# Optimization experiments

Measured on AMD Instinct MI355X. Metric: run time of the kernel, lower is better.

The kernel has to match this reference:

```python
import jax, jax.numpy as jnp
import numpy as np

EPS = 1e-12  # F.normalize default eps


def _sage_conv(x, src, dst, num_nodes, W_l, W_r, b):
    # mean-aggregate neighbor features: for each dst node, mean over x[src]
    agg = jax.ops.segment_sum(x[src], dst, num_segments=num_nodes)  # [N, d_in]
    cnt = jax.ops.segment_sum(jnp.ones((src.shape[0],), x.dtype), dst,
                              num_segments=num_nodes)
    mean = agg / jnp.maximum(cnt, 1.0)[:, None]
    # PyG SAGEConv: lin_l(aggregated) + bias + lin_r(root)
    return mean @ W_l + b + x @ W_r


def setup_inputs() -> dict:
    key = jax.random.key(0)
    ks = jax.random.split(key, 10)
    N, E, F_in = 50000, 400000, 128
    x = jax.random.normal(ks[0], (N, F_in), dtype=jnp.float32)
    edge_index = jax.random.randint(ks[1], (2, E), 0, N, dtype=jnp.int64)

    def lin(k, din, dout):
        s = 1.0 / np.sqrt(din)
        return jax.random.uniform(k, (din, dout), jnp.float32, -s, s)

    params = {
        "W1_l": lin(ks[2], F_in, 2048), "W1_r": lin(ks[3], F_in, 2048),
        "b1": jnp.zeros((2048,), jnp.float32),
        "W2_l": lin(ks[4], 2048, 2048), "W2_r": lin(ks[5], 2048, 2048),
        "b2": jnp.zeros((2048,), jnp.float32),
        "W3_l": lin(ks[6], 2048, 1024), "W3_r": lin(ks[7], 2048, 1024),
        "b3": jnp.zeros((1024,), jnp.float32),
    }
    return {"x": x, "unused": 0, "edge_index": edge_index, **params}


def reference(x, unused, edge_index,
              W1_l, W1_r, b1, W2_l, W2_r, b2, W3_l, W3_r, b3):
    del unused
    N = x.shape[0]
    src, dst = edge_index[0], edge_index[1]
    h = jax.nn.relu(_sage_conv(x, src, dst, N, W1_l, W1_r, b1))
    h = jax.nn.relu(_sage_conv(h, src, dst, N, W2_l, W2_r, b2))
    h = jax.nn.relu(_sage_conv(h, src, dst, N, W3_l, W3_r, b3))
    # F.normalize(dim=1): x / max(||x||_2, eps)
    norm = jnp.linalg.norm(h, axis=1, keepdims=True)
    return h / jnp.maximum(norm, EPS)
```

## Files before the change

### kernel.cpp

```cpp
#include <hip/hip_runtime.h>
#include <stdint.h>

#define NN 50000
#define EE 400000

typedef unsigned short u16;
typedef __attribute__((ext_vector_type(8))) short bf16x8;
typedef __attribute__((ext_vector_type(4))) float f32x4;
typedef __attribute__((address_space(3))) uint32_t lds_u32_t;
typedef __attribute__((address_space(1))) uint32_t glob_u32_t;

__device__ inline float bf2f(u16 u) {
  union { uint32_t i; float f; } x; x.i = ((uint32_t)u) << 16; return x.f;
}
__device__ inline u16 f2bf(float f) {
  union { float f; uint32_t i; } x; x.f = f;
  x.i += 0x7fffu + ((x.i >> 16) & 1u);
  return (u16)(x.i >> 16);
}
__device__ inline void gload_lds16(const void* g, void* l) {
  __builtin_amdgcn_global_load_lds((const glob_u32_t*)g, (lds_u32_t*)l, 16, 0, 0);
}

__global__ void detect_i64(const int* __restrict__ e, int* __restrict__ flag) {
  __shared__ int sh[256];
  int t = threadIdx.x;
  int v = 0;
  for (int i = t; i < 4096; i += 256) v |= e[2 * i + 1];
  sh[t] = v; __syncthreads();
  for (int s = 128; s > 0; s >>= 1) { if (t < s) sh[t] |= sh[t + s]; __syncthreads(); }
  if (t == 0) flag[0] = (sh[0] == 0) ? 1 : 0;
}

__global__ void conv_edges(const int* __restrict__ e, const int* __restrict__ flag,
                           int* __restrict__ src, int* __restrict__ dst) {
  int i = blockIdx.x * 256 + threadIdx.x;
  if (i >= EE) return;
  if (flag[0]) { src[i] = e[2 * i]; dst[i] = e[2 * (EE + i)]; }
  else         { src[i] = e[i];     dst[i] = e[EE + i]; }
}

__global__ void count_edges(const int* __restrict__ dst, int* __restrict__ cnt) {
  int i = blockIdx.x * 256 + threadIdx.x;
  if (i < EE) atomicAdd(&cnt[dst[i]], 1);
}

__global__ void scan_counts(const int* __restrict__ cnt, int* __restrict__ offs,
                            int* __restrict__ cursor) {
  __shared__ int sh[1024];
  __shared__ int carry_sh;
  int tid = threadIdx.x;
  if (tid == 0) carry_sh = 0;
  __syncthreads();
  int nChunks = (NN + 1023) / 1024;
  for (int c = 0; c < nChunks; ++c) {
    int idx = c * 1024 + tid;
    int v = (idx < NN) ? cnt[idx] : 0;
    sh[tid] = v; __syncthreads();
    for (int off = 1; off < 1024; off <<= 1) {
      int t = (tid >= off) ? sh[tid - off] : 0;
      __syncthreads();
      sh[tid] += t;
      __syncthreads();
    }
    int incl = sh[tid];
    int excl = incl - v + carry_sh;
    if (idx < NN) { offs[idx] = excl; cursor[idx] = excl; }
    __syncthreads();
    if (tid == 0) carry_sh += sh[1023];
    __syncthreads();
  }
}

__global__ void fill_buckets(const int* __restrict__ src, const int* __restrict__ dst,
                             int* __restrict__ cursor, int* __restrict__ bucket) {
  int i = blockIdx.x * 256 + threadIdx.x;
  if (i >= EE) return;
  int p = atomicAdd(&cursor[dst[i]], 1);
  bucket[p] = src[i];
}

__global__ void cvt_bf16(const float* __restrict__ in, u16* __restrict__ out, int n4) {
  int i = blockIdx.x * 256 + threadIdx.x;
  if (i >= n4) return;
  float4 v = ((const float4*)in)[i];
  u16 o[4] = { f2bf(v.x), f2bf(v.y), f2bf(v.z), f2bf(v.w) };
  uint2 pack;
  pack.x = (uint32_t)o[0] | ((uint32_t)o[1] << 16);
  pack.y = (uint32_t)o[2] | ((uint32_t)o[3] << 16);
  ((uint2*)out)[i] = pack;
}

__global__ void transposeW(const float* __restrict__ W, u16* __restrict__ Wt,
                           int K, int Nc) {
  __shared__ float tile[32][33];
  int n0 = blockIdx.x * 32, k0 = blockIdx.y * 32;
  int tx = threadIdx.x, ty = threadIdx.y;
  #pragma unroll
  for (int i = 0; i < 4; ++i)
    tile[ty + i * 8][tx] = W[(size_t)(k0 + ty + i * 8) * Nc + n0 + tx];
  __syncthreads();
  #pragma unroll
  for (int i = 0; i < 4; ++i)
    Wt[(size_t)(n0 + ty + i * 8) * K + k0 + tx] = f2bf(tile[tx][ty + i * 8]);
}

template<int D>
__global__ void agg_mean(const u16* __restrict__ h, const int* __restrict__ offs,
                         const int* __restrict__ cnt, const int* __restrict__ bucket,
                         u16* __restrict__ outp) {
  int node = blockIdx.x;
  int t = threadIdx.x;
  int base = t * 8;
  if (base >= D) return;
  int start = offs[node];
  int c = cnt[node];
  float acc[8];
  #pragma unroll
  for (int i = 0; i < 8; ++i) acc[i] = 0.f;
  for (int j = 0; j < c; ++j) {
    int s = bucket[start + j];
    uint4 q = *(const uint4*)(h + (size_t)s * D + base);
    acc[0] += bf2f((u16)(q.x & 0xffff)); acc[1] += bf2f((u16)(q.x >> 16));
    acc[2] += bf2f((u16)(q.y & 0xffff)); acc[3] += bf2f((u16)(q.y >> 16));
    acc[4] += bf2f((u16)(q.z & 0xffff)); acc[5] += bf2f((u16)(q.z >> 16));
    acc[6] += bf2f((u16)(q.w & 0xffff)); acc[7] += bf2f((u16)(q.w >> 16));
  }
  float inv = 1.0f / fmaxf((float)c, 1.0f);
  uint4 o;
  o.x = (uint32_t)f2bf(acc[0] * inv) | ((uint32_t)f2bf(acc[1] * inv) << 16);
  o.y = (uint32_t)f2bf(acc[2] * inv) | ((uint32_t)f2bf(acc[3] * inv) << 16);
  o.z = (uint32_t)f2bf(acc[4] * inv) | ((uint32_t)f2bf(acc[5] * inv) << 16);
  o.w = (uint32_t)f2bf(acc[6] * inv) | ((uint32_t)f2bf(acc[7] * inv) << 16);
  *(uint4*)(outp + (size_t)node * D + base) = o;
}


template<int K>
__device__ inline void stage_half(char* ldsX, const u16* __restrict__ G, int grow0,
                                  int k0, int h, int wave, int lrow8, int slot8,
                                  int clampR) {
  #pragma unroll
  for (int j = 0; j < 2; ++j) {
    const int lrow = h * 128 + j * 64 + wave * 8;
    int gr = grow0 + lrow + lrow8;
    gr = gr < clampR ? gr : clampR - 1;
    gload_lds16(G + (size_t)gr * K + k0 + slot8, ldsX + lrow * 128);
  }
}

#define LOAD_A(MH)                                                              \
  _Pragma("unroll") for (int mf = 0; mf < 4; ++mf) {                            \
    af[mf][0] = *(const bf16x8*)(cA + ((MH) * 128 + mf * 16) * 128 + kc0);      \
    af[mf][1] = *(const bf16x8*)(cA + ((MH) * 128 + mf * 16) * 128 + kc1);      \
  }
#define LOAD_B(DST, NH)                                                         \
  _Pragma("unroll") for (int nf = 0; nf < 2; ++nf) {                            \
    DST[nf][0] = *(const bf16x8*)(cB + ((NH) * 128 + nf * 16) * 128 + kc0);     \
    DST[nf][1] = *(const bf16x8*)(cB + ((NH) * 128 + nf * 16) * 128 + kc1);     \
  }
#define QUAD(MH, BREG, NH)                                                      \
  _Pragma("unroll") for (int mf = 0; mf < 4; ++mf)                              \
  _Pragma("unroll") for (int nf = 0; nf < 2; ++nf) {                            \
    acc[(MH)*4+mf][(NH)*2+nf] = __builtin_amdgcn_mfma_f32_16x16x32_bf16(        \
        af[mf][0], BREG[nf][0], acc[(MH)*4+mf][(NH)*2+nf], 0, 0, 0);            \
    acc[(MH)*4+mf][(NH)*2+nf] = __builtin_amdgcn_mfma_f32_16x16x32_bf16(        \
        af[mf][1], BREG[nf][1], acc[(MH)*4+mf][(NH)*2+nf], 0, 0, 0);            \
  }

template<int K, bool OUT_F32>
__global__ __launch_bounds__(512, 2)
void gemm8ph(const u16* __restrict__ A1, const u16* __restrict__ A2,
             const u16* __restrict__ B1t, const u16* __restrict__ B2t,
             const float* __restrict__ bias, void* __restrict__ Cout,
             int M, int Nc, int tilesN) {
  __shared__ __align__(16) char lds[131072];
  constexpr int NTp = K / 64;
  constexpr int NT = 2 * NTp;

  const int nwg = gridDim.x;
  const int bid = blockIdx.x;
  const int wg = (bid & 7) * (nwg >> 3) + (bid >> 3);
  const int bx = wg % tilesN, by = wg / tilesN;
  const int rowBase = by * 256, colBase = bx * 256;

  const int tid = threadIdx.x;
  const int lane = tid & 63;
  const int wave = tid >> 6;
  const int wm = wave >> 2, wn = wave & 3;
  const int r = lane & 15, kg = lane >> 4;
  const int sw = (r & 7) << 4;
  const int kc0 = (kg * 16) ^ sw;
  const int kc1 = (64 + kg * 16) ^ sw;
  const int slot8 = ((lane & 7) ^ ((lane >> 3) & 7)) * 8;
  const int lrow8 = lane >> 3;

  char* const pA0 = lds + (wm * 64 + r) * 128;
  char* const pB0 = lds + 32768 + (wn * 32 + r) * 128;

  f32x4 acc[8][4];
  #pragma unroll
  for (int m = 0; m < 8; ++m)
    #pragma unroll
    for (int n = 0; n < 4; ++n) acc[m][n] = (f32x4){0.f, 0.f, 0.f, 0.f};

  bf16x8 af[4][2], b0[2][2], b1[2][2];

  stage_half<K>(lds,         A1,  rowBase, 0, 0, wave, lrow8, slot8, M);
  stage_half<K>(lds + 32768, B1t, colBase, 0, 0, wave, lrow8, slot8, Nc);
  stage_half<K>(lds + 32768, B1t, colBase, 0, 1, wave, lrow8, slot8, Nc);
  stage_half<K>(lds,         A1,  rowBase, 0, 1, wave, lrow8, slot8, M);
  asm volatile("s_waitcnt vmcnt(4)" ::: "memory");
  __builtin_amdgcn_s_barrier();

  for (int t = 0; t < NT; ++t) {
    const int cur = t & 1;
    const char* cA = pA0 + cur * 65536;
    const char* cB = pB0 + cur * 65536;
    char* nA = lds + (cur ^ 1) * 65536;
    char* nB = nA + 32768;
    const int vt = (t + 1 < NT) ? t + 1 : NT - 1;
    const u16* sA; const u16* sB; int sk0;
    if (vt >= NTp) { sA = A2; sB = B2t; sk0 = (vt - NTp) * 64; }
    else           { sA = A1; sB = B1t; sk0 = vt * 64; }

    LOAD_A(0); LOAD_B(b0, 0);
    stage_half<K>(nA, sA, rowBase, sk0, 0, wave, lrow8, slot8, M);
    __builtin_amdgcn_s_barrier();
    asm volatile("s_waitcnt lgkmcnt(0)" ::: "memory");
    __builtin_amdgcn_s_setprio(1);
    QUAD(0, b0, 0);
    __builtin_amdgcn_s_setprio(0);
    asm volatile("s_waitcnt vmcnt(4)" ::: "memory");
    __builtin_amdgcn_s_barrier();

    LOAD_B(b1, 1);
    stage_half<K>(nB, sB, colBase, sk0, 0, wave, lrow8, slot8, Nc);
    __builtin_amdgcn_s_barrier();
    asm volatile("s_waitcnt lgkmcnt(0)" ::: "memory");
    __builtin_amdgcn_s_setprio(1);
    QUAD(0, b1, 1);
    __builtin_amdgcn_s_setprio(0);
    asm volatile("s_waitcnt vmcnt(4)" ::: "memory");
    __builtin_amdgcn_s_barrier();

    LOAD_A(1);
    stage_half<K>(nB, sB, colBase, sk0, 1, wave, lrow8, slot8, Nc);
    __builtin_amdgcn_s_barrier();
    asm volatile("s_waitcnt lgkmcnt(0)" ::: "memory");
    __builtin_amdgcn_s_setprio(1);
    QUAD(1, b1, 1);
    __builtin_amdgcn_s_setprio(0);
    __builtin_amdgcn_s_barrier();

    stage_half<K>(nA, sA, rowBase, sk0, 1, wave, lrow8, slot8, M);
    __builtin_amdgcn_s_barrier();
    __builtin_amdgcn_s_setprio(1);
    QUAD(1, b0, 0);
    __builtin_amdgcn_s_setprio(0);
    asm volatile("s_waitcnt vmcnt(4)" ::: "memory");
    __builtin_amdgcn_s_barrier();
  }

  asm volatile("s_waitcnt vmcnt(0)" ::: "memory");

  const int q = lane >> 4;
  #pragma unroll
  for (int m = 0; m < 8; ++m) {
    int row = rowBase + (m >> 2) * 128 + wm * 64 + (m & 3) * 16 + q * 4;
    #pragma unroll
    for (int n = 0; n < 4; ++n) {
      int col = colBase + (n >> 1) * 128 + wn * 32 + (n & 1) * 16 + r;
      float bv = bias[col];
      #pragma unroll
      for (int reg = 0; reg < 4; ++reg) {
        if (row + reg < M) {
          float v = acc[m][n][reg] + bv;
          v = fmaxf(v, 0.f);
          if constexpr (OUT_F32)
            ((float*)Cout)[(size_t)(row + reg) * Nc + col] = v;
          else
            ((u16*)Cout)[(size_t)(row + reg) * Nc + col] = f2bf(v);
        }
      }
    }
  }
}

__global__ void l2norm_rows(float* __restrict__ out) {
  int node = blockIdx.x;
  int t = threadIdx.x;
  float4* p = (float4*)(out + (size_t)node * 1024);
  float4 v = p[t];
  float ss = v.x * v.x + v.y * v.y + v.z * v.z + v.w * v.w;
  #pragma unroll
  for (int off = 32; off > 0; off >>= 1) ss += __shfl_down(ss, off);
  __shared__ float sw[4];
  int lane = t & 63, w = t >> 6;
  if (lane == 0) sw[w] = ss;
  __syncthreads();
  float total = sw[0] + sw[1] + sw[2] + sw[3];
  float scale = 1.0f / fmaxf(sqrtf(total), 1e-12f);
  v.x *= scale; v.y *= scale; v.z *= scale; v.w *= scale;
  p[t] = v;
}

extern "C" void kernel_launch(void* const* d_in, const int* in_sizes, int n_in,
                              void* d_out, int out_size, void* d_ws, size_t ws_size,
                              hipStream_t stream) {
  const float* x   = (const float*)d_in[0];
  const int*   eix = (const int*)d_in[2];
  const float* W1l = (const float*)d_in[3];
  const float* W1r = (const float*)d_in[4];
  const float* b1  = (const float*)d_in[5];
  const float* W2l = (const float*)d_in[6];
  const float* W2r = (const float*)d_in[7];
  const float* b2  = (const float*)d_in[8];
  const float* W3l = (const float*)d_in[9];
  const float* W3r = (const float*)d_in[10];
  const float* b3  = (const float*)d_in[11];

  char* ws = (char*)d_ws;
  size_t off = 0;
  auto alloc = [&](size_t bytes) -> char* {
    char* p = ws + off;
    off += (bytes + 255) & ~(size_t)255;
    return p;
  };
  int* flag   = (int*)alloc(4);
  int* srcA   = (int*)alloc((size_t)EE * 4);
  int* dstA   = (int*)alloc((size_t)EE * 4);
  int* bucket = (int*)alloc((size_t)EE * 4);
  int* cnt    = (int*)alloc((size_t)NN * 4);
  int* offs   = (int*)alloc((size_t)NN * 4);
  int* cursor = (int*)alloc((size_t)NN * 4);
  u16* xb     = (u16*)alloc((size_t)NN * 128 * 2);
  u16* mean1  = (u16*)alloc((size_t)NN * 128 * 2);
  u16* W1lT   = (u16*)alloc((size_t)2048 * 128 * 2);
  u16* W1rT   = (u16*)alloc((size_t)2048 * 128 * 2);
  u16* W2lT   = (u16*)alloc((size_t)2048 * 2048 * 2);
  u16* W2rT   = (u16*)alloc((size_t)2048 * 2048 * 2);
  u16* W3lT   = (u16*)alloc((size_t)1024 * 2048 * 2);
  u16* W3rT   = (u16*)alloc((size_t)1024 * 2048 * 2);
  u16* bufA   = (u16*)alloc((size_t)NN * 2048 * 2);
  u16* bufB   = (u16*)alloc((size_t)NN * 2048 * 2);
  u16* mean2  = (u16*)d_out;

  detect_i64<<<1, 256, 0, stream>>>(eix, flag);
  conv_edges<<<(EE + 255) / 256, 256, 0, stream>>>(eix, flag, srcA, dstA);

  hipMemsetAsync(cnt, 0, (size_t)NN * 4, stream);
  count_edges<<<(EE + 255) / 256, 256, 0, stream>>>(dstA, cnt);
  scan_counts<<<1, 1024, 0, stream>>>(cnt, offs, cursor);
  fill_buckets<<<(EE + 255) / 256, 256, 0, stream>>>(srcA, dstA, cursor, bucket);

  cvt_bf16<<<(NN * 128 / 4 + 255) / 256, 256, 0, stream>>>(x, xb, NN * 128 / 4);
  transposeW<<<dim3(2048 / 32, 128 / 32), dim3(32, 8), 0, stream>>>(W1l, W1lT, 128, 2048);
  transposeW<<<dim3(2048 / 32, 128 / 32), dim3(32, 8), 0, stream>>>(W1r, W1rT, 128, 2048);
  transposeW<<<dim3(2048 / 32, 2048 / 32), dim3(32, 8), 0, stream>>>(W2l, W2lT, 2048, 2048);
  transposeW<<<dim3(2048 / 32, 2048 / 32), dim3(32, 8), 0, stream>>>(W2r, W2rT, 2048, 2048);
  transposeW<<<dim3(1024 / 32, 2048 / 32), dim3(32, 8), 0, stream>>>(W3l, W3lT, 2048, 1024);
  transposeW<<<dim3(1024 / 32, 2048 / 32), dim3(32, 8), 0, stream>>>(W3r, W3rT, 2048, 1024);

  const int tilesM = (NN + 255) / 256;

  agg_mean<128><<<NN, 64, 0, stream>>>(xb, offs, cnt, bucket, mean1);
  gemm8ph<128, false><<<tilesM * 8, 512, 0, stream>>>(
      mean1, xb, W1lT, W1rT, b1, bufA, NN, 2048, 8);

  agg_mean<2048><<<NN, 256, 0, stream>>>(bufA, offs, cnt, bucket, mean2);
  gemm8ph<2048, false><<<tilesM * 8, 512, 0, stream>>>(
      mean2, bufA, W2lT, W2rT, b2, bufB, NN, 2048, 8);

  agg_mean<2048><<<NN, 256, 0, stream>>>(bufB, offs, cnt, bucket, bufA);
  gemm8ph<2048, true><<<tilesM * 4, 512, 0, stream>>>(
      bufA, bufB, W3lT, W3rT, b3, d_out, NN, 1024, 4);

  l2norm_rows<<<NN, 256, 0, stream>>>((float*)d_out);
}
```

Before: 2.175 ms.

## Software-pipeline LDS fragment loads and halve barriers in GEMM main loop

Reorders the 8-phase GEMM loop so that each phase issues its MFMA block first and then the LDS fragment reads for the next phase, plus the next global-to-LDS stage. The first fragments of the next k-tile are prefetched at the end of each iteration, and the prologue preloads the first ones. Barriers per iteration drop from eight to four, vmcnt waits are tightened to 2, and sched_barrier is used to stop the compiler from moving code across phases. The aim is to hide LDS read latency behind MFMA work and cut synchronisation stalls. The cost is more live fragment registers and tighter ordering that could race or spill if the count is off.

```diff
diff --git a/kernel.cpp b/kernel.cpp
--- a/kernel.cpp
+++ b/kernel.cpp
@@ -149,15 +149,15 @@
   }
 }
 
-#define LOAD_A(MH)                                                              \
+#define LOAD_A(BASE, MH)                                                        \
   _Pragma("unroll") for (int mf = 0; mf < 4; ++mf) {                            \
-    af[mf][0] = *(const bf16x8*)(cA + ((MH) * 128 + mf * 16) * 128 + kc0);      \
-    af[mf][1] = *(const bf16x8*)(cA + ((MH) * 128 + mf * 16) * 128 + kc1);      \
-  }
-#define LOAD_B(DST, NH)                                                         \
+    af[mf][0] = *(const bf16x8*)((BASE) + ((MH) * 128 + mf * 16) * 128 + kc0);  \
+    af[mf][1] = *(const bf16x8*)((BASE) + ((MH) * 128 + mf * 16) * 128 + kc1);  \
+  }
+#define LOAD_B(DST, BASE, NH)                                                   \
   _Pragma("unroll") for (int nf = 0; nf < 2; ++nf) {                            \
-    DST[nf][0] = *(const bf16x8*)(cB + ((NH) * 128 + nf * 16) * 128 + kc0);     \
-    DST[nf][1] = *(const bf16x8*)(cB + ((NH) * 128 + nf * 16) * 128 + kc1);     \
+    DST[nf][0] = *(const bf16x8*)((BASE) + ((NH) * 128 + nf * 16) * 128 + kc0); \
+    DST[nf][1] = *(const bf16x8*)((BASE) + ((NH) * 128 + nf * 16) * 128 + kc1); \
   }
 #define QUAD(MH, BREG, NH)                                                      \
   _Pragma("unroll") for (int mf = 0; mf < 4; ++mf)                              \
@@ -167,6 +167,9 @@
     acc[(MH)*4+mf][(NH)*2+nf] = __builtin_amdgcn_mfma_f32_16x16x32_bf16(        \
         af[mf][1], BREG[nf][1], acc[(MH)*4+mf][(NH)*2+nf], 0, 0, 0);            \
   }
+#define PHASE_BAR()                                                             \
+  __builtin_amdgcn_s_barrier();                                                 \
+  __builtin_amdgcn_sched_barrier(0)
 
 template<int K, bool OUT_F32>
 __global__ __launch_bounds__(512, 2)
@@ -210,13 +213,17 @@
   stage_half<K>(lds + 32768, B1t, colBase, 0, 0, wave, lrow8, slot8, Nc);
   stage_half<K>(lds + 32768, B1t, colBase, 0, 1, wave, lrow8, slot8, Nc);
   stage_half<K>(lds,         A1,  rowBase, 0, 1, wave, lrow8, slot8, M);
-  asm volatile("s_waitcnt vmcnt(4)" ::: "memory");
-  __builtin_amdgcn_s_barrier();
+  asm volatile("s_waitcnt vmcnt(2)" ::: "memory");
+  PHASE_BAR();
+  LOAD_A(pA0, 0);
+  LOAD_B(b0, pB0, 0);
 
   for (int t = 0; t < NT; ++t) {
     const int cur = t & 1;
     const char* cA = pA0 + cur * 65536;
     const char* cB = pB0 + cur * 65536;
+    const char* nAr = pA0 + (cur ^ 1) * 65536;
+    const char* nBr = pB0 + (cur ^ 1) * 65536;
     char* nA = lds + (cur ^ 1) * 65536;
     char* nB = nA + 32768;
     const int vt = (t + 1 < NT) ? t + 1 : NT - 1;
@@ -224,42 +231,36 @@
     if (vt >= NTp) { sA = A2; sB = B2t; sk0 = (vt - NTp) * 64; }
     else           { sA = A1; sB = B1t; sk0 = vt * 64; }
 
-    LOAD_A(0); LOAD_B(b0, 0);
-    stage_half<K>(nA, sA, rowBase, sk0, 0, wave, lrow8, slot8, M);
-    __builtin_amdgcn_s_barrier();
-    asm volatile("s_waitcnt lgkmcnt(0)" ::: "memory");
     __builtin_amdgcn_s_setprio(1);
     QUAD(0, b0, 0);
     __builtin_amdgcn_s_setprio(0);
-    asm volatile("s_waitcnt vmcnt(4)" ::: "memory");
-    __builtin_amdgcn_s_barrier();
-
-    LOAD_B(b1, 1);
-    stage_half<K>(nB, sB, colBase, sk0, 0, wave, lrow8, slot8, Nc);
-    __builtin_amdgcn_s_barrier();
-    asm volatile("s_waitcnt lgkmcnt(0)" ::: "memory");
+    LOAD_B(b1, cB, 1);
+    stage_half<K>(nA, sA, rowBase, sk0, 0, wave, lrow8, slot8, M);
+    asm volatile("s_waitcnt vmcnt(2)" ::: "memory");
+    PHASE_BAR();
+
     __builtin_amdgcn_s_setprio(1);
     QUAD(0, b1, 1);
     __builtin_amdgcn_s_setprio(0);
-    asm volatile("s_waitcnt vmcnt(4)" ::: "memory");
-    __builtin_amdgcn_s_barrier();
-
-    LOAD_A(1);
-    stage_half<K>(nB, sB, colBase, sk0, 1, wave, lrow8, slot8, Nc);
-    __builtin_amdgcn_s_barrier();
-    asm volatile("s_waitcnt lgkmcnt(0)" ::: "memory");
+    LOAD_A(cA, 1);
+    stage_half<K>(nB, sB, colBase, sk0, 0, wave, lrow8, slot8, Nc);
+    PHASE_BAR();
+
     __builtin_amdgcn_s_setprio(1);
     QUAD(1, b1, 1);
     __builtin_amdgcn_s_setprio(0);
-    __builtin_amdgcn_s_barrier();
-
-    stage_half<K>(nA, sA, rowBase, sk0, 1, wave, lrow8, slot8, M);
-    __builtin_amdgcn_s_barrier();
+    stage_half<K>(nB, sB, colBase, sk0, 1, wave, lrow8, slot8, Nc);
+    asm volatile("s_waitcnt vmcnt(2)" ::: "memory");
+    PHASE_BAR();
+
     __builtin_amdgcn_s_setprio(1);
     QUAD(1, b0, 0);
     __builtin_amdgcn_s_setprio(0);
-    asm volatile("s_waitcnt vmcnt(4)" ::: "memory");
-    __builtin_amdgcn_s_barrier();
+    LOAD_A(nAr, 0);
+    LOAD_B(b0, nBr, 0);
+    stage_half<K>(nA, sA, rowBase, sk0, 1, wave, lrow8, slot8, M);
+    asm volatile("s_waitcnt vmcnt(2)" ::: "memory");
+    PHASE_BAR();
   }
 
   asm volatile("s_waitcnt vmcnt(0)" ::: "memory");
```

Measured after the change: 2.250 ms. 1.03x slower.

## Reorder last SAGE layer: project before aggregating, fuse bias, ReLU and L2 norm

Applied to the files above, without the earlier changes.

Layer 3 now runs a single GEMM of h against the concatenated [W3_l | W3_r] weights, producing a 2048-wide bf16 projection, and then aggregates the neighbour half of that projection. This relies on the mean commuting with the linear map. The aggregation therefore gathers 1024-wide rows instead of 2048-wide ones. A new agg_add_norm kernel adds the root projection and bias, applies ReLU and L2-normalises each row in one pass, which removes the separate l2norm kernel and the layer-3 mean buffer round trip. The projection is rounded to bf16 before aggregation, which changes rounding slightly. The change also assumes W3lT and W3rT sit contiguously in the workspace.

```diff
diff --git a/kernel.cpp b/kernel.cpp
--- a/kernel.cpp
+++ b/kernel.cpp
@@ -135,6 +135,44 @@
   *(uint4*)(outp + (size_t)node * D + base) = o;
 }
 
+__global__ void agg_add_norm(const u16* __restrict__ Y, const int* __restrict__ offs,
+                             const int* __restrict__ cnt, const int* __restrict__ bucket,
+                             const float* __restrict__ b3, float* __restrict__ outp) {
+  int node = blockIdx.x;
+  int t = threadIdx.x;
+  int base = t * 4;
+  int start = offs[node];
+  int c = cnt[node];
+  float acc[4] = {0.f, 0.f, 0.f, 0.f};
+  for (int j = 0; j < c; ++j) {
+    int s = bucket[start + j];
+    uint2 q = *(const uint2*)(Y + (size_t)s * 2048 + base);
+    acc[0] += bf2f((u16)(q.x & 0xffff)); acc[1] += bf2f((u16)(q.x >> 16));
+    acc[2] += bf2f((u16)(q.y & 0xffff)); acc[3] += bf2f((u16)(q.y >> 16));
+  }
+  float inv = 1.0f / fmaxf((float)c, 1.0f);
+  uint2 qr = *(const uint2*)(Y + (size_t)node * 2048 + 1024 + base);
+  float yr[4] = { bf2f((u16)(qr.x & 0xffff)), bf2f((u16)(qr.x >> 16)),
+                  bf2f((u16)(qr.y & 0xffff)), bf2f((u16)(qr.y >> 16)) };
+  float4 bv = *(const float4*)(b3 + base);
+  float v[4];
+  v[0] = fmaxf(acc[0] * inv + yr[0] + bv.x, 0.f);
+  v[1] = fmaxf(acc[1] * inv + yr[1] + bv.y, 0.f);
+  v[2] = fmaxf(acc[2] * inv + yr[2] + bv.z, 0.f);
+  v[3] = fmaxf(acc[3] * inv + yr[3] + bv.w, 0.f);
+  float ss = v[0] * v[0] + v[1] * v[1] + v[2] * v[2] + v[3] * v[3];
+  #pragma unroll
+  for (int off = 32; off > 0; off >>= 1) ss += __shfl_down(ss, off);
+  __shared__ float sw[4];
+  int lane = t & 63, w = t >> 6;
+  if (lane == 0) sw[w] = ss;
+  __syncthreads();
+  float total = sw[0] + sw[1] + sw[2] + sw[3];
+  float scale = 1.0f / fmaxf(sqrtf(total), 1e-12f);
+  float4 o = { v[0] * scale, v[1] * scale, v[2] * scale, v[3] * scale };
+  *(float4*)(outp + (size_t)node * 1024 + base) = o;
+}
+
 
 template<int K>
 __device__ inline void stage_half(char* ldsX, const u16* __restrict__ G, int grow0,
@@ -168,15 +206,15 @@
         af[mf][1], BREG[nf][1], acc[(MH)*4+mf][(NH)*2+nf], 0, 0, 0);            \
   }
 
-template<int K, bool OUT_F32>
+template<int K, bool DUAL, bool EPI, bool OUT_F32>
 __global__ __launch_bounds__(512, 2)
-void gemm8ph(const u16* __restrict__ A1, const u16* __restrict__ A2,
-             const u16* __restrict__ B1t, const u16* __restrict__ B2t,
-             const float* __restrict__ bias, void* __restrict__ Cout,
-             int M, int Nc, int tilesN) {
+void gemm2src(const u16* __restrict__ A1, const u16* __restrict__ A2,
+              const u16* __restrict__ B1t, const u16* __restrict__ B2t,
+              const float* __restrict__ bias, void* __restrict__ Cout,
+              int M, int Nc, int tilesN) {
   __shared__ __align__(16) char lds[131072];
   constexpr int NTp = K / 64;
-  constexpr int NT = 2 * NTp;
+  constexpr int NT = DUAL ? 2 * NTp : NTp;
 
   const int nwg = gridDim.x;
   const int bid = blockIdx.x;
@@ -221,8 +259,8 @@
     char* nB = nA + 32768;
     const int vt = (t + 1 < NT) ? t + 1 : NT - 1;
     const u16* sA; const u16* sB; int sk0;
-    if (vt >= NTp) { sA = A2; sB = B2t; sk0 = (vt - NTp) * 64; }
-    else           { sA = A1; sB = B1t; sk0 = vt * 64; }
+    if (DUAL && vt >= NTp) { sA = A2; sB = B2t; sk0 = (vt - NTp) * 64; }
+    else                   { sA = A1; sB = B1t; sk0 = vt * 64; }
 
     LOAD_A(0); LOAD_B(b0, 0);
     stage_half<K>(nA, sA, rowBase, sk0, 0, wave, lrow8, slot8, M);
@@ -271,12 +309,12 @@
     #pragma unroll
     for (int n = 0; n < 4; ++n) {
       int col = colBase + (n >> 1) * 128 + wn * 32 + (n & 1) * 16 + r;
-      float bv = bias[col];
+      float bv = EPI ? bias[col] : 0.f;
       #pragma unroll
       for (int reg = 0; reg < 4; ++reg) {
         if (row + reg < M) {
-          float v = acc[m][n][reg] + bv;
-          v = fmaxf(v, 0.f);
+          float v = acc[m][n][reg];
+          if constexpr (EPI) v = fmaxf(v + bv, 0.f);
           if constexpr (OUT_F32)
             ((float*)Cout)[(size_t)(row + reg) * Nc + col] = v;
           else
@@ -285,24 +323,6 @@
       }
     }
   }
-}
-
-__global__ void l2norm_rows(float* __restrict__ out) {
-  int node = blockIdx.x;
-  int t = threadIdx.x;
-  float4* p = (float4*)(out + (size_t)node * 1024);
-  float4 v = p[t];
-  float ss = v.x * v.x + v.y * v.y + v.z * v.z + v.w * v.w;
-  #pragma unroll
-  for (int off = 32; off > 0; off >>= 1) ss += __shfl_down(ss, off);
-  __shared__ float sw[4];
-  int lane = t & 63, w = t >> 6;
-  if (lane == 0) sw[w] = ss;
-  __syncthreads();
-  float total = sw[0] + sw[1] + sw[2] + sw[3];
-  float scale = 1.0f / fmaxf(sqrtf(total), 1e-12f);
-  v.x *= scale; v.y *= scale; v.z *= scale; v.w *= scale;
-  p[t] = v;
 }
 
 extern "C" void kernel_launch(void* const* d_in, const int* in_sizes, int n_in,
@@ -365,16 +385,14 @@
   const int tilesM = (NN + 255) / 256;
 
   agg_mean<128><<<NN, 64, 0, stream>>>(xb, offs, cnt, bucket, mean1);
-  gemm8ph<128, false><<<tilesM * 8, 512, 0, stream>>>(
+  gemm2src<128, true, true, false><<<tilesM * 8, 512, 0, stream>>>(
       mean1, xb, W1lT, W1rT, b1, bufA, NN, 2048, 8);
 
   agg_mean<2048><<<NN, 256, 0, stream>>>(bufA, offs, cnt, bucket, mean2);
-  gemm8ph<2048, false><<<tilesM * 8, 512, 0, stream>>>(
+  gemm2src<2048, true, true, false><<<tilesM * 8, 512, 0, stream>>>(
       mean2, bufA, W2lT, W2rT, b2, bufB, NN, 2048, 8);
 
-  agg_mean<2048><<<NN, 256, 0, stream>>>(bufB, offs, cnt, bucket, bufA);
-  gemm8ph<2048, true><<<tilesM * 4, 512, 0, stream>>>(
-      bufA, bufB, W3lT, W3rT, b3, d_out, NN, 1024, 4);
-
-  l2norm_rows<<<NN, 256, 0, stream>>>((float*)d_out);
-}
+  gemm2src<2048, false, false, false><<<tilesM * 8, 512, 0, stream>>>(
+      bufB, nullptr, W3lT, nullptr, nullptr, bufA, NN, 2048, 8);
+  agg_add_norm<<<NN, 256, 0, stream>>>(bufA, offs, cnt, bucket, b3, (float*)d_out);
+}
```

After: 1.982 ms (median of 2 runs). -8.9%, faster.
